# Performance work log

Hardware: AMD Instinct MI355X
Metric: run time of the kernel (lower is better)

Reference implementation:

```python
import jax, jax.numpy as jnp
import numpy as np

N_MEL = 80
N_CTX = 640  # n_text_channels + n_speaker_dim = 512 + 128
N_ATT = 128
TEMPERATURE = 1.0


def setup_inputs() -> dict:
    key = jax.random.key(0)
    ks = jax.random.split(key, 7)
    Tq, B, Tk = 512, 8, 256
    queries = jax.random.normal(ks[0], (Tq, B, N_MEL), dtype=jnp.float32)
    keys = jax.random.normal(ks[1], (Tk, B, N_CTX), dtype=jnp.float32)
    values = jax.random.normal(ks[2], (Tk, B, N_CTX), dtype=jnp.float32)
    # Linear weights (torch nn.Linear stores W as (out, in); y = x @ W.T)
    sq = 1.0 / np.sqrt(N_MEL)
    sk = 1.0 / np.sqrt(N_CTX)
    sv = 1.0 / np.sqrt(N_ATT)
    Wq = jax.random.normal(ks[3], (N_ATT, N_MEL), dtype=jnp.float32) * sq
    Wk = jax.random.normal(ks[4], (N_ATT, N_CTX), dtype=jnp.float32) * sk
    Wv = jax.random.normal(ks[5], (N_ATT, N_CTX), dtype=jnp.float32) * sk
    Wvec = jax.random.normal(ks[6], (N_ATT,), dtype=jnp.float32) * sv  # v: Linear(N_ATT, 1)
    return {"queries": queries, "keys": keys, "values": values,
            "Wq": Wq, "Wk": Wk, "Wv": Wv, "Wvec": Wvec}


def reference(queries, keys, values, Wq, Wk, Wv, Wvec):
    # Projections then time-major -> batch-major: (T,B,*) -> (B,T,C)
    q = jnp.einsum('tbi,ci->btc', queries, Wq)   # (B, Tq, C)
    k = jnp.einsum('tbi,ci->btc', keys, Wk)      # (B, Tk, C)
    v = jnp.einsum('tbi,ci->btc', values, Wv)    # (B, Tk, C)
    # Additive (Bahdanau) energies: broadcast add + tanh + v-dot reduce
    energy = jnp.tanh(q[:, :, None, :] + k[:, None, :, :])  # (B, Tq, Tk, C)
    attn = jnp.einsum('bqkc,c->bqk', energy, Wvec) / TEMPERATURE
    attn = jax.nn.softmax(attn, axis=2)          # softmax over Tk
    out = jnp.einsum('bqk,bkc->bqc', attn, v)    # (B, Tq, C)
    out = jnp.transpose(out, (0, 2, 1))          # (B, C, Tq)
    return (out, attn)
```

## Files before the change

kernel.cpp:

```cpp
#include <hip/hip_runtime.h>

#define TQ 512
#define TK 256
#define BB 8
#define CC 128

#define SCALE2L2E 2.8853900817779268f
#define L2E 1.4426950408889634f

__device__ __forceinline__ float fexp2(float x) { return __builtin_amdgcn_exp2f(x); }
__device__ __forceinline__ float frcp(float x)  { return __builtin_amdgcn_rcpf(x); }

typedef __fp16 h16x2 __attribute__((ext_vector_type(2)));
typedef __fp16 h16x4 __attribute__((ext_vector_type(4)));
typedef __fp16 h16x8 __attribute__((ext_vector_type(8)));
typedef _Float16 f16x8 __attribute__((ext_vector_type(8)));
typedef float f32x4 __attribute__((ext_vector_type(4)));

__device__ __forceinline__ f16x8 pack8(float4 lo, float4 hi) {
    h16x2 a0 = __builtin_amdgcn_cvt_pkrtz(lo.x, lo.y);
    h16x2 a1 = __builtin_amdgcn_cvt_pkrtz(lo.z, lo.w);
    h16x2 a2 = __builtin_amdgcn_cvt_pkrtz(hi.x, hi.y);
    h16x2 a3 = __builtin_amdgcn_cvt_pkrtz(hi.z, hi.w);
    h16x4 p0 = __builtin_shufflevector(a0, a1, 0, 1, 2, 3);
    h16x4 p1 = __builtin_shufflevector(a2, a3, 0, 1, 2, 3);
    h16x8 r = __builtin_shufflevector(p0, p1, 0, 1, 2, 3, 4, 5, 6, 7);
    return __builtin_bit_cast(f16x8, r);
}

__device__ __forceinline__ h16x4 pack4h(float4 v) {
    h16x2 lo = __builtin_amdgcn_cvt_pkrtz(v.x, v.y);
    h16x2 hi = __builtin_amdgcn_cvt_pkrtz(v.z, v.w);
    return __builtin_shufflevector(lo, hi, 0, 1, 2, 3);
}

#define CWK 10240
#define CWV 10240
#define CWQ 1536
#define CXQ 49152
#define CXK 163840
#define CXV 163840
#define CTOT (CWK + CWV + CWQ + CXQ + CXK + CXV)

__global__ __launch_bounds__(256) void convert_kernel(
    const float* __restrict__ Wk, const float* __restrict__ Wv,
    const float* __restrict__ Wq, const float* __restrict__ q_in,
    const float* __restrict__ k_in, const float* __restrict__ v_in,
    f16x8* __restrict__ Wk16s, f16x8* __restrict__ Wv16s,
    f16x8* __restrict__ Wq16s, f16x8* __restrict__ Xq16s,
    f16x8* __restrict__ Xk16s, f16x8* __restrict__ Xv16s)
{
    const int d = blockIdx.x * 256 + threadIdx.x;
    if (d >= CTOT) return;
    const f16x8 zero = {};

    const float* __restrict__ src;
    f16x8* __restrict__ dst;
    int dd, K;
    if (d < CWK)                         { dd = d; src = Wk; dst = Wk16s; K = 640; }
    else if (d < CWK + CWV)              { dd = d - CWK; src = Wv; dst = Wv16s; K = 640; }
    else if (d < CWK + CWV + CWQ)        { dd = d - CWK - CWV; src = Wq; dst = Wq16s; K = 80; }
    else if (d < CWK + CWV + CWQ + CXQ)  { dd = d - CWK - CWV - CWQ; src = q_in; dst = Xq16s; K = 80; }
    else if (d < CTOT - CXV)             { dd = d - CWK - CWV - CWQ - CXQ; src = k_in; dst = Xk16s; K = 640; }
    else                                 { dd = d - (CTOT - CXV); src = v_in; dst = Xv16s; K = 640; }

    const int nstep = (K == 640) ? 20 : 3;
    const int per = nstep * 64;
    const int tile = dd / per, rem = dd % per;
    const int s = rem >> 6, l = rem & 63;
    const int lr = l & 15, lk = l >> 4;
    const int r = tile * 16 + lr, k0 = s * 32 + lk * 8;
    if (K == 80 && k0 >= 80) { dst[dd] = zero; return; }
    float4 lo = *(const float4*)&src[(size_t)r * K + k0];
    float4 hi = *(const float4*)&src[(size_t)r * K + k0 + 4];
    dst[dd] = pack8(lo, hi);
}

__global__ __launch_bounds__(256) void proj_mfma(
    const _Float16* __restrict__ Wk16s, const _Float16* __restrict__ Wv16s,
    const _Float16* __restrict__ Wq16s, const _Float16* __restrict__ Xq16s,
    const _Float16* __restrict__ Xk16s, const _Float16* __restrict__ Xv16s,
    float* __restrict__ eqp, float* __restrict__ ekp, _Float16* __restrict__ v16s)
{
    const int tid = threadIdx.x;
    const int w = tid >> 6;
    const int l = tid & 63;
    const int lr = l & 15, lk = l >> 4;
    const int id = blockIdx.x;
    const int j = (id >> 1) * 4 + w;

    f32x4 acc0 = {0.f, 0.f, 0.f, 0.f};
    f32x4 acc1 = {0.f, 0.f, 0.f, 0.f};

    if ((id & 1) == 0) {
        const int tensor = j >> 9;
        const int jj = j & 511;
        const int rtile = jj >> 2;
        const int c0 = (jj & 3) * 32;
        const int r0 = rtile * 16;
        const _Float16* __restrict__ Xs = tensor ? Xv16s : Xk16s;
        const _Float16* __restrict__ Wt = tensor ? Wv16s : Wk16s;

        const _Float16* __restrict__ A0 = Xs + (size_t)rtile * 10240 + l * 8;
        const _Float16* __restrict__ B0 = Wt + (c0 >> 4) * 10240 + l * 8;
        const _Float16* __restrict__ B1 = B0 + 10240;

#pragma unroll
        for (int s = 0; s < 20; ++s) {
            f16x8 a = *(const f16x8*)(A0 + s * 512);
            f16x8 b0 = *(const f16x8*)(B0 + s * 512);
            f16x8 b1 = *(const f16x8*)(B1 + s * 512);
            acc0 = __builtin_amdgcn_mfma_f32_16x16x32_f16(a, b0, acc0, 0, 0, 0);
            acc1 = __builtin_amdgcn_mfma_f32_16x16x32_f16(a, b1, acc1, 0, 0, 0);
        }

        if (tensor == 0) {
#pragma unroll
            for (int jr = 0; jr < 4; ++jr) {
                int r = r0 + lk * 4 + jr;
                int t = r >> 3, bt = r & 7;
                ekp[((size_t)bt * CC + c0 + lr) * TK + t] = fexp2(SCALE2L2E * acc0[jr]);
                ekp[((size_t)bt * CC + c0 + 16 + lr) * TK + t] = fexp2(SCALE2L2E * acc1[jr]);
            }
        } else {
#pragma unroll
            for (int jr = 0; jr < 4; ++jr) {
                int r = r0 + lk * 4 + jr;
                int t = r >> 3, bt = r & 7;
                int base = bt * 32768 + (t >> 5) * 512 + ((t >> 3) & 3) * 128
                         + lr * 8 + (t & 7);
                v16s[base + (c0 >> 4) * 4096] = (_Float16)acc0[jr];
                v16s[base + ((c0 >> 4) + 1) * 4096] = (_Float16)acc1[jr];
            }
        }
    } else {
        const int rtile = j >> 2;
        const int c0 = (j & 3) * 32;

        const _Float16* __restrict__ A0 = Xq16s + (size_t)rtile * 1536 + l * 8;
        const _Float16* __restrict__ B0 = Wq16s + (c0 >> 4) * 1536 + l * 8;
        const _Float16* __restrict__ B1 = B0 + 1536;

#pragma unroll
        for (int s = 0; s < 3; ++s) {
            f16x8 a = *(const f16x8*)(A0 + s * 512);
            f16x8 bb0 = *(const f16x8*)(B0 + s * 512);
            f16x8 bb1 = *(const f16x8*)(B1 + s * 512);
            acc0 = __builtin_amdgcn_mfma_f32_16x16x32_f16(a, bb0, acc0, 0, 0, 0);
            acc1 = __builtin_amdgcn_mfma_f32_16x16x32_f16(a, bb1, acc1, 0, 0, 0);
        }

#pragma unroll
        for (int jr = 0; jr < 4; ++jr) {
            int r = rtile * 16 + lk * 4 + jr;
            int t = r >> 3, bt = r & 7;
            eqp[((size_t)bt * TQ + t) * CC + c0 + lr] = fexp2(SCALE2L2E * acc0[jr]);
            eqp[((size_t)bt * TQ + t) * CC + c0 + 16 + lr] = fexp2(SCALE2L2E * acc1[jr]);
        }
    }
}

__global__ __launch_bounds__(256) void attn_pv_kernel(
    const float* __restrict__ eqp, const float* __restrict__ ekp,
    const float* __restrict__ Wvec, const _Float16* __restrict__ v16s,
    float* __restrict__ attn_out, float* __restrict__ out)
{
    __shared__ _Float16 pl[16][264];

    const int tid = threadIdx.x;
    const int lane = tid & 63;
    const int w = __builtin_amdgcn_readfirstlane(tid >> 6);
    const int b = blockIdx.y;
    const int q0g = blockIdx.x * 16;
    const int q0 = q0g + w * 4;

    const float* __restrict__ qr0 = eqp + ((size_t)b * TQ + q0) * CC;
    const float* __restrict__ qr1 = qr0 + CC;
    const float* __restrict__ qr2 = qr1 + CC;
    const float* __restrict__ qr3 = qr2 + CC;
    const float* __restrict__ kb = ekp + (size_t)b * CC * TK + lane * 4;

    float sw = Wvec[lane] + Wvec[64 + lane];
#pragma unroll
    for (int m = 32; m >= 1; m >>= 1) sw += __shfl_xor(sw, m, 64);

    float a0[4] = {0.f, 0.f, 0.f, 0.f};
    float a1[4] = {0.f, 0.f, 0.f, 0.f};
    float a2[4] = {0.f, 0.f, 0.f, 0.f};
    float a3[4] = {0.f, 0.f, 0.f, 0.f};

    float4 k0 = *(const float4*)&kb[0 * TK];
    float4 k1 = *(const float4*)&kb[1 * TK];
    float4 k2 = *(const float4*)&kb[2 * TK];
    float4 k3 = *(const float4*)&kb[3 * TK];
    float4 wv = *(const float4*)&Wvec[0];
    float4 qa = *(const float4*)&qr0[0];
    float4 qb = *(const float4*)&qr1[0];
    float4 qc = *(const float4*)&qr2[0];
    float4 qd = *(const float4*)&qr3[0];

    for (int c4 = 0; c4 < CC; c4 += 4) {
        float4 n0, n1, n2, n3, nwv, nqa, nqb, nqc, nqd;
        if (c4 + 4 < CC) {
            n0 = *(const float4*)&kb[(c4 + 4) * TK];
            n1 = *(const float4*)&kb[(c4 + 5) * TK];
            n2 = *(const float4*)&kb[(c4 + 6) * TK];
            n3 = *(const float4*)&kb[(c4 + 7) * TK];
            nwv = *(const float4*)&Wvec[c4 + 4];
            nqa = *(const float4*)&qr0[c4 + 4];
            nqb = *(const float4*)&qr1[c4 + 4];
            nqc = *(const float4*)&qr2[c4 + 4];
            nqd = *(const float4*)&qr3[c4 + 4];
        }
#define CCOMP(KF, WW, EA, EB, EC, ED)                                   \
        a0[0] = fmaf(WW, frcp(fmaf(EA, KF.x, 1.f)), a0[0]);             \
        a0[1] = fmaf(WW, frcp(fmaf(EA, KF.y, 1.f)), a0[1]);             \
        a0[2] = fmaf(WW, frcp(fmaf(EA, KF.z, 1.f)), a0[2]);             \
        a0[3] = fmaf(WW, frcp(fmaf(EA, KF.w, 1.f)), a0[3]);             \
        a1[0] = fmaf(WW, frcp(fmaf(EB, KF.x, 1.f)), a1[0]);             \
        a1[1] = fmaf(WW, frcp(fmaf(EB, KF.y, 1.f)), a1[1]);             \
        a1[2] = fmaf(WW, frcp(fmaf(EB, KF.z, 1.f)), a1[2]);             \
        a1[3] = fmaf(WW, frcp(fmaf(EB, KF.w, 1.f)), a1[3]);             \
        a2[0] = fmaf(WW, frcp(fmaf(EC, KF.x, 1.f)), a2[0]);             \
        a2[1] = fmaf(WW, frcp(fmaf(EC, KF.y, 1.f)), a2[1]);             \
        a2[2] = fmaf(WW, frcp(fmaf(EC, KF.z, 1.f)), a2[2]);             \
        a2[3] = fmaf(WW, frcp(fmaf(EC, KF.w, 1.f)), a2[3]);             \
        a3[0] = fmaf(WW, frcp(fmaf(ED, KF.x, 1.f)), a3[0]);             \
        a3[1] = fmaf(WW, frcp(fmaf(ED, KF.y, 1.f)), a3[1]);             \
        a3[2] = fmaf(WW, frcp(fmaf(ED, KF.z, 1.f)), a3[2]);             \
        a3[3] = fmaf(WW, frcp(fmaf(ED, KF.w, 1.f)), a3[3]);
        CCOMP(k0, wv.x, qa.x, qb.x, qc.x, qd.x)
        CCOMP(k1, wv.y, qa.y, qb.y, qc.y, qd.y)
        CCOMP(k2, wv.z, qa.z, qb.z, qc.z, qd.z)
        CCOMP(k3, wv.w, qa.w, qb.w, qc.w, qd.w)
#undef CCOMP
        k0 = n0; k1 = n1; k2 = n2; k3 = n3;
        wv = nwv; qa = nqa; qb = nqb; qc = nqc; qd = nqd;
    }

    float sc0[4], sc1[4], sc2[4], sc3[4];
#pragma unroll
    for (int j = 0; j < 4; ++j) {
        sc0[j] = sw - 2.f * a0[j];
        sc1[j] = sw - 2.f * a1[j];
        sc2[j] = sw - 2.f * a2[j];
        sc3[j] = sw - 2.f * a3[j];
    }

    float m0 = fmaxf(fmaxf(sc0[0], sc0[1]), fmaxf(sc0[2], sc0[3]));
    float m1 = fmaxf(fmaxf(sc1[0], sc1[1]), fmaxf(sc1[2], sc1[3]));
    float m2 = fmaxf(fmaxf(sc2[0], sc2[1]), fmaxf(sc2[2], sc2[3]));
    float m3 = fmaxf(fmaxf(sc3[0], sc3[1]), fmaxf(sc3[2], sc3[3]));
#pragma unroll
    for (int m = 32; m >= 1; m >>= 1) {
        m0 = fmaxf(m0, __shfl_xor(m0, m, 64));
        m1 = fmaxf(m1, __shfl_xor(m1, m, 64));
        m2 = fmaxf(m2, __shfl_xor(m2, m, 64));
        m3 = fmaxf(m3, __shfl_xor(m3, m, 64));
    }
    float e0[4], e1[4], e2[4], e3[4];
    float s0 = 0.f, s1 = 0.f, s2 = 0.f, s3 = 0.f;
#pragma unroll
    for (int j = 0; j < 4; ++j) {
        e0[j] = fexp2((sc0[j] - m0) * L2E); s0 += e0[j];
        e1[j] = fexp2((sc1[j] - m1) * L2E); s1 += e1[j];
        e2[j] = fexp2((sc2[j] - m2) * L2E); s2 += e2[j];
        e3[j] = fexp2((sc3[j] - m3) * L2E); s3 += e3[j];
    }
#pragma unroll
    for (int m = 32; m >= 1; m >>= 1) {
        s0 += __shfl_xor(s0, m, 64);
        s1 += __shfl_xor(s1, m, 64);
        s2 += __shfl_xor(s2, m, 64);
        s3 += __shfl_xor(s3, m, 64);
    }
    const float r0 = frcp(s0), r1 = frcp(s1), r2 = frcp(s2), r3 = frcp(s3);

    const float4 p0 = make_float4(e0[0] * r0, e0[1] * r0, e0[2] * r0, e0[3] * r0);
    const float4 p1 = make_float4(e1[0] * r1, e1[1] * r1, e1[2] * r1, e1[3] * r1);
    const float4 p2 = make_float4(e2[0] * r2, e2[1] * r2, e2[2] * r2, e2[3] * r2);
    const float4 p3 = make_float4(e3[0] * r3, e3[1] * r3, e3[2] * r3, e3[3] * r3);

    float* __restrict__ po = attn_out + ((size_t)b * TQ + q0) * TK + lane * 4;
    *(float4*)(po + 0 * TK) = p0;
    *(float4*)(po + 1 * TK) = p1;
    *(float4*)(po + 2 * TK) = p2;
    *(float4*)(po + 3 * TK) = p3;

    *(h16x4*)&pl[w * 4 + 0][lane * 4] = pack4h(p0);
    *(h16x4*)&pl[w * 4 + 1][lane * 4] = pack4h(p1);
    *(h16x4*)&pl[w * 4 + 2][lane * 4] = pack4h(p2);
    *(h16x4*)&pl[w * 4 + 3][lane * 4] = pack4h(p3);
    __syncthreads();

    const int lr = lane & 15, lk = lane >> 4;
#pragma unroll
    for (int ct = 0; ct < 2; ++ct) {
        const int ctile = w + ct * 4;
        const _Float16* __restrict__ Vr = v16s + b * 32768 + ctile * 4096 + lane * 8;
        f32x4 acc = {0.f, 0.f, 0.f, 0.f};
#pragma unroll
        for (int s = 0; s < 8; ++s) {
            f16x8 a = *(const f16x8*)&pl[lr][s * 32 + lk * 8];
            f16x8 bv = *(const f16x8*)(Vr + s * 512);
            acc = __builtin_amdgcn_mfma_f32_16x16x32_f16(a, bv, acc, 0, 0, 0);
        }
        float4 o = make_float4(acc[0], acc[1], acc[2], acc[3]);
        *(float4*)&out[((size_t)b * CC + ctile * 16 + lr) * TQ + q0g + lk * 4] = o;
    }
}

extern "C" void kernel_launch(void* const* d_in, const int* in_sizes, int n_in,
                              void* d_out, int out_size, void* d_ws, size_t ws_size,
                              hipStream_t stream) {
    const float* queries = (const float*)d_in[0];
    const float* keys    = (const float*)d_in[1];
    const float* values  = (const float*)d_in[2];
    const float* Wq      = (const float*)d_in[3];
    const float* Wk      = (const float*)d_in[4];
    const float* Wv      = (const float*)d_in[5];
    const float* Wvec    = (const float*)d_in[6];

    float* out  = (float*)d_out;
    float* attn = out + BB * CC * TQ;

    float* ws = (float*)d_ws;
    float* eqp = ws;
    float* ekp = eqp + 4096 * CC;
    _Float16* v16s = (_Float16*)(ekp + 2048 * CC);
    _Float16* Wk16s = v16s + 8 * 32768;
    _Float16* Wv16s = Wk16s + 81920;
    _Float16* Wq16s = Wv16s + 81920;
    _Float16* Xq16s = Wq16s + 12288;
    _Float16* Xk16s = Xq16s + 393216;
    _Float16* Xv16s = Xk16s + 1310720;

    convert_kernel<<<dim3((CTOT + 255) / 256), 256, 0, stream>>>(
        Wk, Wv, Wq, queries, keys, values,
        (f16x8*)Wk16s, (f16x8*)Wv16s, (f16x8*)Wq16s,
        (f16x8*)Xq16s, (f16x8*)Xk16s, (f16x8*)Xv16s);
    proj_mfma<<<dim3(512), 256, 0, stream>>>(
        Wk16s, Wv16s, Wq16s, Xq16s, Xk16s, Xv16s, eqp, ekp, v16s);
    attn_pv_kernel<<<dim3(32, 8), 256, 0, stream>>>(
        eqp, ekp, Wvec, v16s, attn, out);
}
```

Baseline: 47.66 us.

## Split attention channel reduction across two waves per query group

Doubles the attention block to 512 threads and splits the 128-channel energy reduction between two waves, each handling 64 channels. The partial sums are combined through shared memory before softmax, and each of the 8 waves now computes one output channel tile in the PV matmul. The aim is more wave-level parallelism on the grid of 256 blocks, which is under-occupied. The cost is an extra LDS exchange, an additional barrier, and half the waves sitting idle during the softmax.

```diff
diff --git a/kernel.cpp b/kernel.cpp
--- a/kernel.cpp
+++ b/kernel.cpp
@@ -160,25 +160,29 @@
     }
 }
 
-__global__ __launch_bounds__(256) void attn_pv_kernel(
+__global__ __launch_bounds__(512, 2) void attn_pv_kernel(
     const float* __restrict__ eqp, const float* __restrict__ ekp,
     const float* __restrict__ Wvec, const _Float16* __restrict__ v16s,
     float* __restrict__ attn_out, float* __restrict__ out)
 {
+    __shared__ float pa[4][64][17];
     __shared__ _Float16 pl[16][264];
 
     const int tid = threadIdx.x;
     const int lane = tid & 63;
     const int w = __builtin_amdgcn_readfirstlane(tid >> 6);
+    const int g = w >> 1;
+    const int h = w & 1;
     const int b = blockIdx.y;
     const int q0g = blockIdx.x * 16;
-    const int q0 = q0g + w * 4;
-
-    const float* __restrict__ qr0 = eqp + ((size_t)b * TQ + q0) * CC;
+    const int q0 = q0g + g * 4;
+
+    const float* __restrict__ qr0 = eqp + ((size_t)b * TQ + q0) * CC + h * 64;
     const float* __restrict__ qr1 = qr0 + CC;
     const float* __restrict__ qr2 = qr1 + CC;
     const float* __restrict__ qr3 = qr2 + CC;
-    const float* __restrict__ kb = ekp + (size_t)b * CC * TK + lane * 4;
+    const float* __restrict__ kb = ekp + (size_t)b * CC * TK + (h * 64) * TK + lane * 4;
+    const float* __restrict__ wvp = Wvec + h * 64;
 
     float sw = Wvec[lane] + Wvec[64 + lane];
 #pragma unroll
@@ -193,20 +197,20 @@
     float4 k1 = *(const float4*)&kb[1 * TK];
     float4 k2 = *(const float4*)&kb[2 * TK];
     float4 k3 = *(const float4*)&kb[3 * TK];
-    float4 wv = *(const float4*)&Wvec[0];
+    float4 wv = *(const float4*)&wvp[0];
     float4 qa = *(const float4*)&qr0[0];
     float4 qb = *(const float4*)&qr1[0];
     float4 qc = *(const float4*)&qr2[0];
     float4 qd = *(const float4*)&qr3[0];
 
-    for (int c4 = 0; c4 < CC; c4 += 4) {
+    for (int c4 = 0; c4 < 64; c4 += 4) {
         float4 n0, n1, n2, n3, nwv, nqa, nqb, nqc, nqd;
-        if (c4 + 4 < CC) {
+        if (c4 + 4 < 64) {
             n0 = *(const float4*)&kb[(c4 + 4) * TK];
             n1 = *(const float4*)&kb[(c4 + 5) * TK];
             n2 = *(const float4*)&kb[(c4 + 6) * TK];
             n3 = *(const float4*)&kb[(c4 + 7) * TK];
-            nwv = *(const float4*)&Wvec[c4 + 4];
+            nwv = *(const float4*)&wvp[c4 + 4];
             nqa = *(const float4*)&qr0[c4 + 4];
             nqb = *(const float4*)&qr1[c4 + 4];
             nqc = *(const float4*)&qr2[c4 + 4];
@@ -238,76 +242,93 @@
         wv = nwv; qa = nqa; qb = nqb; qc = nqc; qd = nqd;
     }
 
-    float sc0[4], sc1[4], sc2[4], sc3[4];
-#pragma unroll
-    for (int j = 0; j < 4; ++j) {
-        sc0[j] = sw - 2.f * a0[j];
-        sc1[j] = sw - 2.f * a1[j];
-        sc2[j] = sw - 2.f * a2[j];
-        sc3[j] = sw - 2.f * a3[j];
-    }
-
-    float m0 = fmaxf(fmaxf(sc0[0], sc0[1]), fmaxf(sc0[2], sc0[3]));
-    float m1 = fmaxf(fmaxf(sc1[0], sc1[1]), fmaxf(sc1[2], sc1[3]));
-    float m2 = fmaxf(fmaxf(sc2[0], sc2[1]), fmaxf(sc2[2], sc2[3]));
-    float m3 = fmaxf(fmaxf(sc3[0], sc3[1]), fmaxf(sc3[2], sc3[3]));
-#pragma unroll
-    for (int m = 32; m >= 1; m >>= 1) {
-        m0 = fmaxf(m0, __shfl_xor(m0, m, 64));
-        m1 = fmaxf(m1, __shfl_xor(m1, m, 64));
-        m2 = fmaxf(m2, __shfl_xor(m2, m, 64));
-        m3 = fmaxf(m3, __shfl_xor(m3, m, 64));
-    }
-    float e0[4], e1[4], e2[4], e3[4];
-    float s0 = 0.f, s1 = 0.f, s2 = 0.f, s3 = 0.f;
-#pragma unroll
-    for (int j = 0; j < 4; ++j) {
-        e0[j] = fexp2((sc0[j] - m0) * L2E); s0 += e0[j];
-        e1[j] = fexp2((sc1[j] - m1) * L2E); s1 += e1[j];
-        e2[j] = fexp2((sc2[j] - m2) * L2E); s2 += e2[j];
-        e3[j] = fexp2((sc3[j] - m3) * L2E); s3 += e3[j];
-    }
-#pragma unroll
-    for (int m = 32; m >= 1; m >>= 1) {
-        s0 += __shfl_xor(s0, m, 64);
-        s1 += __shfl_xor(s1, m, 64);
-        s2 += __shfl_xor(s2, m, 64);
-        s3 += __shfl_xor(s3, m, 64);
-    }
-    const float r0 = frcp(s0), r1 = frcp(s1), r2 = frcp(s2), r3 = frcp(s3);
-
-    const float4 p0 = make_float4(e0[0] * r0, e0[1] * r0, e0[2] * r0, e0[3] * r0);
-    const float4 p1 = make_float4(e1[0] * r1, e1[1] * r1, e1[2] * r1, e1[3] * r1);
-    const float4 p2 = make_float4(e2[0] * r2, e2[1] * r2, e2[2] * r2, e2[3] * r2);
-    const float4 p3 = make_float4(e3[0] * r3, e3[1] * r3, e3[2] * r3, e3[3] * r3);
-
-    float* __restrict__ po = attn_out + ((size_t)b * TQ + q0) * TK + lane * 4;
-    *(float4*)(po + 0 * TK) = p0;
-    *(float4*)(po + 1 * TK) = p1;
-    *(float4*)(po + 2 * TK) = p2;
-    *(float4*)(po + 3 * TK) = p3;
-
-    *(h16x4*)&pl[w * 4 + 0][lane * 4] = pack4h(p0);
-    *(h16x4*)&pl[w * 4 + 1][lane * 4] = pack4h(p1);
-    *(h16x4*)&pl[w * 4 + 2][lane * 4] = pack4h(p2);
-    *(h16x4*)&pl[w * 4 + 3][lane * 4] = pack4h(p3);
+    if (h == 1) {
+#pragma unroll
+        for (int jj = 0; jj < 4; ++jj) {
+            pa[g][lane][jj]      = a0[jj];
+            pa[g][lane][4 + jj]  = a1[jj];
+            pa[g][lane][8 + jj]  = a2[jj];
+            pa[g][lane][12 + jj] = a3[jj];
+        }
+    }
     __syncthreads();
 
+    if (h == 0) {
+#pragma unroll
+        for (int jj = 0; jj < 4; ++jj) {
+            a0[jj] += pa[g][lane][jj];
+            a1[jj] += pa[g][lane][4 + jj];
+            a2[jj] += pa[g][lane][8 + jj];
+            a3[jj] += pa[g][lane][12 + jj];
+        }
+
+        float sc0[4], sc1[4], sc2[4], sc3[4];
+#pragma unroll
+        for (int j = 0; j < 4; ++j) {
+            sc0[j] = sw - 2.f * a0[j];
+            sc1[j] = sw - 2.f * a1[j];
+            sc2[j] = sw - 2.f * a2[j];
+            sc3[j] = sw - 2.f * a3[j];
+        }
+
+        float m0 = fmaxf(fmaxf(sc0[0], sc0[1]), fmaxf(sc0[2], sc0[3]));
+        float m1 = fmaxf(fmaxf(sc1[0], sc1[1]), fmaxf(sc1[2], sc1[3]));
+        float m2 = fmaxf(fmaxf(sc2[0], sc2[1]), fmaxf(sc2[2], sc2[3]));
+        float m3 = fmaxf(fmaxf(sc3[0], sc3[1]), fmaxf(sc3[2], sc3[3]));
+#pragma unroll
+        for (int m = 32; m >= 1; m >>= 1) {
+            m0 = fmaxf(m0, __shfl_xor(m0, m, 64));
+            m1 = fmaxf(m1, __shfl_xor(m1, m, 64));
+            m2 = fmaxf(m2, __shfl_xor(m2, m, 64));
+            m3 = fmaxf(m3, __shfl_xor(m3, m, 64));
+        }
+        float e0[4], e1[4], e2[4], e3[4];
+        float s0 = 0.f, s1 = 0.f, s2 = 0.f, s3 = 0.f;
+#pragma unroll
+        for (int j = 0; j < 4; ++j) {
+            e0[j] = fexp2((sc0[j] - m0) * L2E); s0 += e0[j];
+            e1[j] = fexp2((sc1[j] - m1) * L2E); s1 += e1[j];
+            e2[j] = fexp2((sc2[j] - m2) * L2E); s2 += e2[j];
+            e3[j] = fexp2((sc3[j] - m3) * L2E); s3 += e3[j];
+        }
+#pragma unroll
+        for (int m = 32; m >= 1; m >>= 1) {
+            s0 += __shfl_xor(s0, m, 64);
+            s1 += __shfl_xor(s1, m, 64);
+            s2 += __shfl_xor(s2, m, 64);
+            s3 += __shfl_xor(s3, m, 64);
+        }
+        const float r0 = frcp(s0), r1 = frcp(s1), r2 = frcp(s2), r3 = frcp(s3);
+
+        const float4 p0 = make_float4(e0[0] * r0, e0[1] * r0, e0[2] * r0, e0[3] * r0);
+        const float4 p1 = make_float4(e1[0] * r1, e1[1] * r1, e1[2] * r1, e1[3] * r1);
+        const float4 p2 = make_float4(e2[0] * r2, e2[1] * r2, e2[2] * r2, e2[3] * r2);
+        const float4 p3 = make_float4(e3[0] * r3, e3[1] * r3, e3[2] * r3, e3[3] * r3);
+
+        float* __restrict__ po = attn_out + ((size_t)b * TQ + q0) * TK + lane * 4;
+        *(float4*)(po + 0 * TK) = p0;
+        *(float4*)(po + 1 * TK) = p1;
+        *(float4*)(po + 2 * TK) = p2;
+        *(float4*)(po + 3 * TK) = p3;
+
+        *(h16x4*)&pl[g * 4 + 0][lane * 4] = pack4h(p0);
+        *(h16x4*)&pl[g * 4 + 1][lane * 4] = pack4h(p1);
+        *(h16x4*)&pl[g * 4 + 2][lane * 4] = pack4h(p2);
+        *(h16x4*)&pl[g * 4 + 3][lane * 4] = pack4h(p3);
+    }
+    __syncthreads();
+
     const int lr = lane & 15, lk = lane >> 4;
-#pragma unroll
-    for (int ct = 0; ct < 2; ++ct) {
-        const int ctile = w + ct * 4;
-        const _Float16* __restrict__ Vr = v16s + b * 32768 + ctile * 4096 + lane * 8;
-        f32x4 acc = {0.f, 0.f, 0.f, 0.f};
-#pragma unroll
-        for (int s = 0; s < 8; ++s) {
-            f16x8 a = *(const f16x8*)&pl[lr][s * 32 + lk * 8];
-            f16x8 bv = *(const f16x8*)(Vr + s * 512);
-            acc = __builtin_amdgcn_mfma_f32_16x16x32_f16(a, bv, acc, 0, 0, 0);
-        }
-        float4 o = make_float4(acc[0], acc[1], acc[2], acc[3]);
-        *(float4*)&out[((size_t)b * CC + ctile * 16 + lr) * TQ + q0g + lk * 4] = o;
-    }
+    const _Float16* __restrict__ Vr = v16s + b * 32768 + w * 4096 + lane * 8;
+    f32x4 acc = {0.f, 0.f, 0.f, 0.f};
+#pragma unroll
+    for (int s = 0; s < 8; ++s) {
+        f16x8 a = *(const f16x8*)&pl[lr][s * 32 + lk * 8];
+        f16x8 bv = *(const f16x8*)(Vr + s * 512);
+        acc = __builtin_amdgcn_mfma_f32_16x16x32_f16(a, bv, acc, 0, 0, 0);
+    }
+    float4 o = make_float4(acc[0], acc[1], acc[2], acc[3]);
+    *(float4*)&out[((size_t)b * CC + w * 16 + lr) * TQ + q0g + lk * 4] = o;
 }
 
 extern "C" void kernel_launch(void* const* d_in, const int* in_sizes, int n_in,
@@ -341,6 +362,6 @@
         (f16x8*)Xq16s, (f16x8*)Xk16s, (f16x8*)Xv16s);
     proj_mfma<<<dim3(512), 256, 0, stream>>>(
         Wk16s, Wv16s, Wq16s, Xq16s, Xk16s, Xv16s, eqp, ekp, v16s);
-    attn_pv_kernel<<<dim3(32, 8), 256, 0, stream>>>(
+    attn_pv_kernel<<<dim3(32, 8), 512, 0, stream>>>(
         eqp, ekp, Wvec, v16s, attn, out);
 }
```

Result: faster. 40.93 us (median of 2 runs) (-14.1%).
